# Optimization experiments

Measured on AMD Instinct MI355X. Metric: run time of the kernel, lower is better.

The kernel has to match this reference:

```python
import jax, jax.numpy as jnp
import numpy as np

HIGHEST = jax.lax.Precision.HIGHEST
KEY_CHUNK_SIZE = 4096 * 4  # hard-coded in the module's __call__
HEADS = 8
DIM_HEAD = 64


def _query_chunk_size(num_q: int) -> int:
    # replicates the module's static chunk-size selection
    if num_q % 64 == 0:
        return num_q // 64
    if num_q % 16 == 0:
        return num_q // 16
    if num_q % 4 == 0:
        return num_q // 4
    return num_q


def _me_attention(q, k, v, q_chunk: int, k_chunk: int):
    # q, k, v: (S, H, D) where H here is the flattened batch*heads axis
    S, H, D = q.shape
    num_kv = k.shape[0]
    k_chunk = min(k_chunk, num_kv)
    q = q / jnp.sqrt(jnp.asarray(D, q.dtype))
    kc = k.reshape(-1, k_chunk, H, D)          # (nk, kc, H, D)
    vc = v.reshape(-1, k_chunk, H, v.shape[-1])

    def per_qchunk(qch):  # qch: (qc, H, D)
        def summarize(args):
            kch, vch = args
            s = jnp.einsum('qhd,khd->qhk', qch, kch, precision=HIGHEST)
            m = jax.lax.stop_gradient(jnp.max(s, axis=-1, keepdims=True))
            e = jnp.exp(s - m)
            ev = jnp.einsum('khf,qhk->qhf', vch, e, precision=HIGHEST)
            return ev, e.sum(axis=-1), m[..., 0]
        evs, ews, ms = jax.lax.map(summarize, (kc, vc))  # stacked over key chunks
        gm = jnp.max(ms, axis=0)                # (qc, H) global running max
        sc = jnp.exp(ms - gm)                   # (nk, qc, H) rescale factors
        num = (evs * sc[..., None]).sum(axis=0)
        den = (ews * sc).sum(axis=0)
        return num / den[..., None]

    qs = q.reshape(-1, q_chunk, H, D)
    out = jax.lax.map(per_qchunk, qs)           # (nq, qc, H, F)
    return out.reshape(S, H, -1)


def _forward(hidden_states, w_q, w_k, w_v, w_out, b_out):
    B, S, Dm = hidden_states.shape
    H, dh = HEADS, DIM_HEAD
    q = hidden_states @ w_q
    k = hidden_states @ w_k
    v = hidden_states @ w_v

    def to_heads(t):  # (B,S,H*dh) -> (B*H, S, dh)
        return t.reshape(B, S, H, dh).transpose(0, 2, 1, 3).reshape(B * H, S, dh)

    qs, ks, vs = to_heads(q), to_heads(k), to_heads(v)
    # module transposes to (S, B*H, dh) before memory-efficient attention
    qcs = _query_chunk_size(S)
    attn = _me_attention(qs.transpose(1, 0, 2), ks.transpose(1, 0, 2),
                         vs.transpose(1, 0, 2), qcs, KEY_CHUNK_SIZE)
    attn = attn.transpose(1, 0, 2)  # (B*H, S, dh)
    attn = attn.reshape(B, H, S, dh).transpose(0, 2, 1, 3).reshape(B, S, H * dh)
    return attn @ w_out + b_out


def setup_inputs() -> dict:
    key = jax.random.key(0)
    ks = jax.random.split(key, 6)
    B, S, Dm = 2, 8192, 512
    inner = HEADS * DIM_HEAD  # 512
    return {
        'hidden_states': jax.random.normal(ks[0], (B, S, Dm), dtype=jnp.float32),
        'w_q': jax.random.normal(ks[1], (Dm, inner), dtype=jnp.float32) * 0.02,
        'w_k': jax.random.normal(ks[2], (Dm, inner), dtype=jnp.float32) * 0.02,
        'w_v': jax.random.normal(ks[3], (Dm, inner), dtype=jnp.float32) * 0.02,
        'w_out': jax.random.normal(ks[4], (inner, Dm), dtype=jnp.float32) * 0.02,
        'b_out': jnp.zeros((Dm,), dtype=jnp.float32),
    }


def reference(hidden_states, w_q, w_k, w_v, w_out, b_out):
    return _forward(hidden_states, w_q, w_k, w_v, w_out, b_out)
```

## Files before the change

### kernel.cpp

```cpp
#include <hip/hip_runtime.h>
#include <stdint.h>

typedef unsigned short u16;
typedef __attribute__((ext_vector_type(8))) short short8;
typedef __attribute__((ext_vector_type(4))) short short4v;
typedef __attribute__((ext_vector_type(4))) float f32x4;

#define MFMA16(a, b, c) __builtin_amdgcn_mfma_f32_16x16x16bf16_1k(a, b, c, 0, 0, 0)
#define MFMA32(a, b, c) __builtin_amdgcn_mfma_f32_16x16x32_bf16(a, b, c, 0, 0, 0)

#if __has_builtin(__builtin_amdgcn_exp2f)
#define EXP2F(x) __builtin_amdgcn_exp2f(x)
#else
#define EXP2F(x) exp2f(x)
#endif

#define ASYNC16(G, L)                                                            \
    __builtin_amdgcn_global_load_lds((const __attribute__((address_space(1))) void*)(const void*)(G), \
                                     (__attribute__((address_space(3))) void*)(void*)(L), 16, 0, 0)

__device__ __forceinline__ u16 f2bf(float f) {
    union { float f; uint32_t u; } c; c.f = f;
    uint32_t r = (c.u + 0x7fffu + ((c.u >> 16) & 1u)) >> 16;
    return (u16)r;
}

__global__ __launch_bounds__(256) void k_convert_x(const float* __restrict__ X, u16* __restrict__ Xb) {
    int idx = blockIdx.x * 256 + threadIdx.x;
    float4 v = ((const float4*)X)[idx];
    union { u16 s[4]; uint2 v; } u;
    u.s[0] = f2bf(v.x); u.s[1] = f2bf(v.y); u.s[2] = f2bf(v.z); u.s[3] = f2bf(v.w);
    ((uint2*)Xb)[idx] = u.v;
}

__global__ __launch_bounds__(256) void k_convert_w(const float* __restrict__ W0, const float* __restrict__ W1,
                                                   const float* __restrict__ W2, const float* __restrict__ W3,
                                                   u16* __restrict__ Wt) {
    __shared__ u16 T[64][72];
    const float* W = (blockIdx.z == 0) ? W0 : (blockIdx.z == 1) ? W1 : (blockIdx.z == 2) ? W2 : W3;
    int k0 = blockIdx.x * 64, n0 = blockIdx.y * 64;
    int t = threadIdx.x;
    for (int i = 0; i < 4; i++) {
        int id = t + i * 256;
        int row = id >> 4, c4 = (id & 15) * 4;
        float4 v = *(const float4*)(W + (size_t)(k0 + row) * 512 + n0 + c4);
        union { u16 s[4]; uint2 v; } u;
        u.s[0] = f2bf(v.x); u.s[1] = f2bf(v.y); u.s[2] = f2bf(v.z); u.s[3] = f2bf(v.w);
        *(uint2*)&T[row][c4] = u.v;
    }
    __syncthreads();
    u16* O = Wt + (size_t)blockIdx.z * 512 * 512;
    for (int i = 0; i < 2; i++) {
        int id = t + i * 256;
        int row = id >> 3, c8 = (id & 7) * 8;
        union { u16 s[8]; uint4 v; } tmp;
        for (int j = 0; j < 8; j++) tmp.s[j] = T[c8 + j][row];
        *(uint4*)(O + (size_t)(n0 + row) * 512 + k0 + c8) = tmp.v;
    }
}

__global__ __launch_bounds__(256) void k_gemm_qkv(const u16* __restrict__ X, const u16* __restrict__ Wt,
                                                  u16* __restrict__ Q, u16* __restrict__ K, u16* __restrict__ V) {
    __shared__ u16 As[128][40];
    __shared__ u16 Bs[128][40];
    const int t = threadIdx.x;
    const int wave = t >> 6, lane = t & 63, quad = lane >> 4, l16 = lane & 15;
    const int wm = (wave >> 1) * 64, wn = (wave & 1) * 64;
    const int m0 = blockIdx.x * 128, n0 = blockIdx.y * 128;
    const u16* Bt = Wt + (size_t)blockIdx.z * 262144;
    const f32x4 fz = {0.f, 0.f, 0.f, 0.f};
    f32x4 acc[4][4];
    for (int i = 0; i < 4; i++) for (int j = 0; j < 4; j++) acc[i][j] = fz;
    for (int k0 = 0; k0 < 512; k0 += 32) {
        __syncthreads();
        for (int i = 0; i < 2; i++) {
            int id = t + i * 256;
            int row = id >> 2, c8 = (id & 3) * 8;
            *(uint4*)&As[row][c8] = *(const uint4*)(X + (size_t)(m0 + row) * 512 + k0 + c8);
            *(uint4*)&Bs[row][c8] = *(const uint4*)(Bt + (size_t)(n0 + row) * 512 + k0 + c8);
        }
        __syncthreads();
        short8 af[4], bf[4];
        for (int mt = 0; mt < 4; mt++) af[mt] = *(const short8*)&As[wm + mt * 16 + l16][quad * 8];
        for (int nt = 0; nt < 4; nt++) bf[nt] = *(const short8*)&Bs[wn + nt * 16 + l16][quad * 8];
        for (int mt = 0; mt < 4; mt++)
            for (int nt = 0; nt < 4; nt++)
                acc[mt][nt] = MFMA32(af[mt], bf[nt], acc[mt][nt]);
    }
    const float scale = (blockIdx.z == 0) ? 0.18033688011112042f : 1.0f;
    u16* Out = (blockIdx.z == 0) ? Q : (blockIdx.z == 1) ? K : V;
    for (int mt = 0; mt < 4; mt++)
        for (int nt = 0; nt < 4; nt++)
            for (int r = 0; r < 4; r++) {
                int m = m0 + wm + mt * 16 + quad * 4 + r;
                int n = n0 + wn + nt * 16 + l16;
                int b = m >> 13, s = m & 8191, h = n >> 6, d = n & 63;
                Out[((size_t)((b * 8 + h) * 8192 + s)) * 64 + d] = f2bf(acc[mt][nt][r] * scale);
            }
}

__global__ __launch_bounds__(256) void k_transpose_v(const u16* __restrict__ V, u16* __restrict__ Vt) {
    __shared__ u16 T[64][72];
    int s0 = blockIdx.x * 64, bh = blockIdx.y;
    int t = threadIdx.x;
    for (int i = 0; i < 2; i++) {
        int id = t + i * 256, row = id >> 3, c8 = (id & 7) * 8;
        *(uint4*)&T[row][c8] = *(const uint4*)(V + ((size_t)bh * 8192 + s0 + row) * 64 + c8);
    }
    __syncthreads();
    for (int i = 0; i < 2; i++) {
        int id = t + i * 256, row = id >> 3, c8 = (id & 7) * 8;
        union { u16 s[8]; uint4 v; } tmp;
        for (int j = 0; j < 8; j++) tmp.s[j] = T[c8 + j][row];
        *(uint4*)(Vt + ((size_t)bh * 64 + row) * 8192 + s0 + c8) = tmp.v;
    }
}

__global__ __launch_bounds__(512, 4) void k_flash(const u16* __restrict__ Q, const u16* __restrict__ K,
                                                  const u16* __restrict__ Vt, u16* __restrict__ Attn) {
    __shared__ u16 KsAll[2][4096];
    __shared__ u16 VsAll[2][4096];
    const int t = threadIdx.x;
    const int wave = t >> 6, lane = t & 63, quad = lane >> 4, l16 = lane & 15;
    const int l7 = l16 & 7, q1 = quad >> 1, qlo = quad & 1;
    const int qblk = blockIdx.x, bh = blockIdx.y;
    const int b = bh >> 3, h = bh & 7;
    const int q0g = qblk * 256;
    const int mq = wave * 32;
    const u16* Qb = Q + ((size_t)bh * 8192 + q0g) * 64;
    const u16* Kb = K + (size_t)bh * 8192 * 64;
    const u16* Vb = Vt + (size_t)bh * 64 * 8192;

    const int r0 = t >> 3;
    const int x0 = ((t & 7) ^ (r0 & 7)) * 8;
    const u16* gK0 = Kb + r0 * 64 + x0;
    const u16* gV0 = Vb + (size_t)r0 * 8192 + x0;
    u16* lK = &KsAll[0][0] + t * 8;
    u16* lV = &VsAll[0][0] + t * 8;

    auto prefetch = [&](int it, int buf) {
        ASYNC16(gK0 + it * 4096, lK + buf * 4096);
        ASYNC16(gV0 + it * 64,   lV + buf * 4096);
    };

    short8 qf[2][2];
    for (int mt = 0; mt < 2; mt++)
        for (int ks = 0; ks < 2; ks++)
            qf[mt][ks] = *(const short8*)(Qb + (size_t)(mq + mt * 16 + l16) * 64 + ks * 32 + quad * 8);

    const f32x4 fz = {0.f, 0.f, 0.f, 0.f};
    f32x4 o[2][4];
    float l_i[2] = {0.f, 0.f};
    for (int mt = 0; mt < 2; mt++) for (int nt = 0; nt < 4; nt++) o[mt][nt] = fz;

    prefetch(0, 0);

    auto body = [&](int it, int buf) {
        __syncthreads();
        if (it != 127) prefetch(it + 1, buf ^ 1);
        const u16* KsB = &KsAll[buf][0];
        const u16* VsB = &VsAll[buf][0];

        f32x4 sc[2][4];
        for (int kt = 0; kt < 4; kt++) {
            short8 kf0 = *(const short8*)(KsB + kt * 1024 + l16 * 64 + (((0 * 4 + quad) ^ l7) * 8));
            short8 kf1 = *(const short8*)(KsB + kt * 1024 + l16 * 64 + (((1 * 4 + quad) ^ l7) * 8));
            sc[0][kt] = MFMA32(kf0, qf[0][0], fz);
            sc[1][kt] = MFMA32(kf0, qf[1][0], fz);
            sc[0][kt] = MFMA32(kf1, qf[0][1], sc[0][kt]);
            sc[1][kt] = MFMA32(kf1, qf[1][1], sc[1][kt]);
        }

        short4v pf[2][4];
        for (int mt = 0; mt < 2; mt++)
            for (int kt = 0; kt < 4; kt++) {
                union { float f; uint32_t u; } e0, e1, e2, e3;
                e0.f = EXP2F(sc[mt][kt][0]);
                e1.f = EXP2F(sc[mt][kt][1]);
                e2.f = EXP2F(sc[mt][kt][2]);
                e3.f = EXP2F(sc[mt][kt][3]);
                l_i[mt] += (e0.f + e1.f) + (e2.f + e3.f);
                union { uint32_t u[2]; short4v s; } pk;
                pk.u[0] = __builtin_amdgcn_perm(e1.u, e0.u, 0x07060302);
                pk.u[1] = __builtin_amdgcn_perm(e3.u, e2.u, 0x07060302);
                pf[mt][kt] = pk.s;
            }

        for (int kt = 0; kt < 4; kt++)
            for (int nt = 0; nt < 4; nt++) {
                short4v vf = *(const short4v*)(VsB + nt * 1024 + l16 * 64 + (((kt * 2 + q1) ^ l7) * 8) + qlo * 4);
                o[0][nt] = MFMA16(pf[0][kt], vf, o[0][nt]);
                o[1][nt] = MFMA16(pf[1][kt], vf, o[1][nt]);
            }
    };

    for (int it2 = 0; it2 < 64; it2++) {
        body(2 * it2, 0);
        body(2 * it2 + 1, 1);
    }

    for (int mt = 0; mt < 2; mt++) {
        float l = l_i[mt];
        l += __shfl_xor(l, 16);
        l += __shfl_xor(l, 32);
        float inv = 1.0f / l;
        float invC[4];
        for (int r = 0; r < 4; r++) invC[r] = __shfl(inv, quad * 4 + r);
        for (int nt = 0; nt < 4; nt++)
            for (int r = 0; r < 4; r++) {
                int sg = q0g + mq + mt * 16 + quad * 4 + r;
                int n = h * 64 + nt * 16 + l16;
                Attn[((size_t)(b * 8192 + sg)) * 512 + n] = f2bf(o[mt][nt][r] * invC[r]);
            }
    }
}

__global__ __launch_bounds__(256) void k_gemm_out(const u16* __restrict__ A, const u16* __restrict__ Wot,
                                                  const float* __restrict__ bias, float* __restrict__ Out) {
    __shared__ u16 As[128][40];
    __shared__ u16 Bs[128][40];
    const int t = threadIdx.x;
    const int wave = t >> 6, lane = t & 63, quad = lane >> 4, l16 = lane & 15;
    const int wm = (wave >> 1) * 64, wn = (wave & 1) * 64;
    const int m0 = blockIdx.x * 128, n0 = blockIdx.y * 128;
    const f32x4 fz = {0.f, 0.f, 0.f, 0.f};
    f32x4 acc[4][4];
    for (int i = 0; i < 4; i++) for (int j = 0; j < 4; j++) acc[i][j] = fz;
    for (int k0 = 0; k0 < 512; k0 += 32) {
        __syncthreads();
        for (int i = 0; i < 2; i++) {
            int id = t + i * 256;
            int row = id >> 2, c8 = (id & 3) * 8;
            *(uint4*)&As[row][c8] = *(const uint4*)(A + (size_t)(m0 + row) * 512 + k0 + c8);
            *(uint4*)&Bs[row][c8] = *(const uint4*)(Wot + (size_t)(n0 + row) * 512 + k0 + c8);
        }
        __syncthreads();
        short8 af[4], bf[4];
        for (int mt = 0; mt < 4; mt++) af[mt] = *(const short8*)&As[wm + mt * 16 + l16][quad * 8];
        for (int nt = 0; nt < 4; nt++) bf[nt] = *(const short8*)&Bs[wn + nt * 16 + l16][quad * 8];
        for (int mt = 0; mt < 4; mt++)
            for (int nt = 0; nt < 4; nt++)
                acc[mt][nt] = MFMA32(af[mt], bf[nt], acc[mt][nt]);
    }
    float bv[4];
    for (int nt = 0; nt < 4; nt++) bv[nt] = bias[n0 + wn + nt * 16 + l16];
    for (int mt = 0; mt < 4; mt++)
        for (int nt = 0; nt < 4; nt++)
            for (int r = 0; r < 4; r++) {
                int m = m0 + wm + mt * 16 + quad * 4 + r;
                int n = n0 + wn + nt * 16 + l16;
                Out[(size_t)m * 512 + n] = acc[mt][nt][r] + bv[nt];
            }
}

extern "C" void kernel_launch(void* const* d_in, const int* in_sizes, int n_in,
                              void* d_out, int out_size, void* d_ws, size_t ws_size,
                              hipStream_t stream) {
    const float* X   = (const float*)d_in[0];
    const float* w_q = (const float*)d_in[1];
    const float* w_k = (const float*)d_in[2];
    const float* w_v = (const float*)d_in[3];
    const float* w_o = (const float*)d_in[4];
    const float* b_o = (const float*)d_in[5];
    float* Out = (float*)d_out;

    char* ws = (char*)d_ws;
    u16* Xb   = (u16*)(ws);
    u16* Wt   = (u16*)(ws + 16777216);
    u16* Qd   = (u16*)(ws + 18874368);
    u16* Kd   = (u16*)(ws + 35651584);
    u16* Vd   = (u16*)(ws + 52428800);
    u16* Vtd  = (u16*)(ws + 69206016);
    u16* Attn = Xb;

    hipLaunchKernelGGL(k_convert_x, dim3(8192), dim3(256), 0, stream, X, Xb);
    hipLaunchKernelGGL(k_convert_w, dim3(8, 8, 4), dim3(256), 0, stream, w_q, w_k, w_v, w_o, Wt);
    hipLaunchKernelGGL(k_gemm_qkv, dim3(128, 4, 3), dim3(256), 0, stream, Xb, Wt, Qd, Kd, Vd);
    hipLaunchKernelGGL(k_transpose_v, dim3(128, 16), dim3(256), 0, stream, Vd, Vtd);
    hipLaunchKernelGGL(k_flash, dim3(32, 16), dim3(512), 0, stream, Qd, Kd, Vtd, Attn);
    hipLaunchKernelGGL(k_gemm_out, dim3(128, 4), dim3(256), 0, stream, Attn, Wt + 3 * 262144, b_o, Out);
}
```

Baseline: 437.5 us.

## Use 16x16x32 bf16 MFMA for PV product via permuted K row mapping

Permutes the key rows assigned to each QK^T score tile and changes the K LDS swizzle so each lane's exponentiated scores form a contiguous 8-element bf16 fragment. That lets the P·V product use the K=32 MFMA with 128-bit V loads, halving the MFMA instruction count and the V LDS reads for that stage. In exchange it adds more complex row-index arithmetic and needs the K swizzle and the score layout to agree exactly.

```diff
diff --git a/kernel.cpp b/kernel.cpp
--- a/kernel.cpp
+++ b/kernel.cpp
@@ -122,7 +122,7 @@
     __shared__ u16 VsAll[2][4096];
     const int t = threadIdx.x;
     const int wave = t >> 6, lane = t & 63, quad = lane >> 4, l16 = lane & 15;
-    const int l7 = l16 & 7, q1 = quad >> 1, qlo = quad & 1;
+    const int l7 = l16 & 7;
     const int qblk = blockIdx.x, bh = blockIdx.y;
     const int b = bh >> 3, h = bh & 7;
     const int q0g = qblk * 256;
@@ -131,10 +131,13 @@
     const u16* Kb = K + (size_t)bh * 8192 * 64;
     const u16* Vb = Vt + (size_t)bh * 64 * 8192;
 
+    const int rA = ((l16 & 12) << 1) + (l16 & 3);
+
     const int r0 = t >> 3;
-    const int x0 = ((t & 7) ^ (r0 & 7)) * 8;
-    const u16* gK0 = Kb + r0 * 64 + x0;
-    const u16* gV0 = Vb + (size_t)r0 * 8192 + x0;
+    const int x0K = ((t & 7) ^ ((r0 & 3) | ((r0 & 8) >> 1))) * 8;
+    const int x0V = ((t & 7) ^ (r0 & 7)) * 8;
+    const u16* gK0 = Kb + r0 * 64 + x0K;
+    const u16* gV0 = Vb + (size_t)r0 * 8192 + x0V;
     u16* lK = &KsAll[0][0] + t * 8;
     u16* lV = &VsAll[0][0] + t * 8;
 
@@ -161,36 +164,50 @@
         const u16* KsB = &KsAll[buf][0];
         const u16* VsB = &VsAll[buf][0];
 
-        f32x4 sc[2][4];
-        for (int kt = 0; kt < 4; kt++) {
-            short8 kf0 = *(const short8*)(KsB + kt * 1024 + l16 * 64 + (((0 * 4 + quad) ^ l7) * 8));
-            short8 kf1 = *(const short8*)(KsB + kt * 1024 + l16 * 64 + (((1 * 4 + quad) ^ l7) * 8));
-            sc[0][kt] = MFMA32(kf0, qf[0][0], fz);
-            sc[1][kt] = MFMA32(kf0, qf[1][0], fz);
-            sc[0][kt] = MFMA32(kf1, qf[0][1], sc[0][kt]);
-            sc[1][kt] = MFMA32(kf1, qf[1][1], sc[1][kt]);
+        f32x4 scA[2][2], scB[2][2];
+        for (int kg = 0; kg < 2; kg++) {
+            const u16* KgA = KsB + kg * 2048 + rA * 64;
+            const u16* KgB = KgA + 4 * 64;
+            short8 a0 = *(const short8*)(KgA + ((0 * 4 + quad) ^ l7) * 8);
+            short8 a1 = *(const short8*)(KgA + ((1 * 4 + quad) ^ l7) * 8);
+            short8 b0 = *(const short8*)(KgB + ((0 * 4 + quad) ^ l7) * 8);
+            short8 b1 = *(const short8*)(KgB + ((1 * 4 + quad) ^ l7) * 8);
+            scA[0][kg] = MFMA32(a0, qf[0][0], fz);
+            scA[1][kg] = MFMA32(a0, qf[1][0], fz);
+            scB[0][kg] = MFMA32(b0, qf[0][0], fz);
+            scB[1][kg] = MFMA32(b0, qf[1][0], fz);
+            scA[0][kg] = MFMA32(a1, qf[0][1], scA[0][kg]);
+            scA[1][kg] = MFMA32(a1, qf[1][1], scA[1][kg]);
+            scB[0][kg] = MFMA32(b1, qf[0][1], scB[0][kg]);
+            scB[1][kg] = MFMA32(b1, qf[1][1], scB[1][kg]);
         }
 
-        short4v pf[2][4];
+        short8 pf[2][2];
         for (int mt = 0; mt < 2; mt++)
-            for (int kt = 0; kt < 4; kt++) {
-                union { float f; uint32_t u; } e0, e1, e2, e3;
-                e0.f = EXP2F(sc[mt][kt][0]);
-                e1.f = EXP2F(sc[mt][kt][1]);
-                e2.f = EXP2F(sc[mt][kt][2]);
-                e3.f = EXP2F(sc[mt][kt][3]);
-                l_i[mt] += (e0.f + e1.f) + (e2.f + e3.f);
-                union { uint32_t u[2]; short4v s; } pk;
-                pk.u[0] = __builtin_amdgcn_perm(e1.u, e0.u, 0x07060302);
-                pk.u[1] = __builtin_amdgcn_perm(e3.u, e2.u, 0x07060302);
-                pf[mt][kt] = pk.s;
-            }
-
-        for (int kt = 0; kt < 4; kt++)
+            for (int kg = 0; kg < 2; kg++) {
+                union { float f; uint32_t u; } eA0, eA1, eA2, eA3, eB0, eB1, eB2, eB3;
+                eA0.f = EXP2F(scA[mt][kg][0]);
+                eA1.f = EXP2F(scA[mt][kg][1]);
+                eA2.f = EXP2F(scA[mt][kg][2]);
+                eA3.f = EXP2F(scA[mt][kg][3]);
+                eB0.f = EXP2F(scB[mt][kg][0]);
+                eB1.f = EXP2F(scB[mt][kg][1]);
+                eB2.f = EXP2F(scB[mt][kg][2]);
+                eB3.f = EXP2F(scB[mt][kg][3]);
+                l_i[mt] += ((eA0.f + eA1.f) + (eA2.f + eA3.f)) + ((eB0.f + eB1.f) + (eB2.f + eB3.f));
+                union { uint32_t u[4]; short8 s; } pk;
+                pk.u[0] = __builtin_amdgcn_perm(eA1.u, eA0.u, 0x07060302);
+                pk.u[1] = __builtin_amdgcn_perm(eA3.u, eA2.u, 0x07060302);
+                pk.u[2] = __builtin_amdgcn_perm(eB1.u, eB0.u, 0x07060302);
+                pk.u[3] = __builtin_amdgcn_perm(eB3.u, eB2.u, 0x07060302);
+                pf[mt][kg] = pk.s;
+            }
+
+        for (int kg = 0; kg < 2; kg++)
             for (int nt = 0; nt < 4; nt++) {
-                short4v vf = *(const short4v*)(VsB + nt * 1024 + l16 * 64 + (((kt * 2 + q1) ^ l7) * 8) + qlo * 4);
-                o[0][nt] = MFMA16(pf[0][kt], vf, o[0][nt]);
-                o[1][nt] = MFMA16(pf[1][kt], vf, o[1][nt]);
+                short8 vf = *(const short8*)(VsB + nt * 1024 + l16 * 64 + (((kg * 4 + quad) ^ l7) * 8));
+                o[0][nt] = MFMA32(pf[0][kg], vf, o[0][nt]);
+                o[1][nt] = MFMA32(pf[1][kg], vf, o[1][nt]);
             }
     };
 
```

New measurement: 392.2 us. -10.3%, faster.

## Switch flash attention to 32x32 MFMA tiles and fuse X conversion into QKV GEMM

Applied to the files above, without the earlier changes.

The flash kernel now uses 32x32x16 bf16 MFMAs for both QK^T and PV instead of 16x16 tiles. The K load order is permuted so the score accumulator layout can be packed straight into PV operands without shuffles, and the epilogue is rewritten for the 32x32 layout. Separately, the fp32-to-bf16 conversion of X moves into the QKV GEMM's LDS load, which removes one kernel launch and a round trip through memory. The cost is that X is reread and converted again for each N tile and each of the three projections.

```diff
diff --git a/kernel.cpp b/kernel.cpp
--- a/kernel.cpp
+++ b/kernel.cpp
@@ -3,11 +3,11 @@
 
 typedef unsigned short u16;
 typedef __attribute__((ext_vector_type(8))) short short8;
-typedef __attribute__((ext_vector_type(4))) short short4v;
 typedef __attribute__((ext_vector_type(4))) float f32x4;
-
-#define MFMA16(a, b, c) __builtin_amdgcn_mfma_f32_16x16x16bf16_1k(a, b, c, 0, 0, 0)
+typedef __attribute__((ext_vector_type(16))) float f32x16;
+
 #define MFMA32(a, b, c) __builtin_amdgcn_mfma_f32_16x16x32_bf16(a, b, c, 0, 0, 0)
+#define MFMA3232(a, b, c) __builtin_amdgcn_mfma_f32_32x32x16_bf16(a, b, c, 0, 0, 0)
 
 #if __has_builtin(__builtin_amdgcn_exp2f)
 #define EXP2F(x) __builtin_amdgcn_exp2f(x)
@@ -23,14 +23,6 @@
     union { float f; uint32_t u; } c; c.f = f;
     uint32_t r = (c.u + 0x7fffu + ((c.u >> 16) & 1u)) >> 16;
     return (u16)r;
-}
-
-__global__ __launch_bounds__(256) void k_convert_x(const float* __restrict__ X, u16* __restrict__ Xb) {
-    int idx = blockIdx.x * 256 + threadIdx.x;
-    float4 v = ((const float4*)X)[idx];
-    union { u16 s[4]; uint2 v; } u;
-    u.s[0] = f2bf(v.x); u.s[1] = f2bf(v.y); u.s[2] = f2bf(v.z); u.s[3] = f2bf(v.w);
-    ((uint2*)Xb)[idx] = u.v;
 }
 
 __global__ __launch_bounds__(256) void k_convert_w(const float* __restrict__ W0, const float* __restrict__ W1,
@@ -59,7 +51,7 @@
     }
 }
 
-__global__ __launch_bounds__(256) void k_gemm_qkv(const u16* __restrict__ X, const u16* __restrict__ Wt,
+__global__ __launch_bounds__(256) void k_gemm_qkv(const float* __restrict__ X, const u16* __restrict__ Wt,
                                                   u16* __restrict__ Q, u16* __restrict__ K, u16* __restrict__ V) {
     __shared__ u16 As[128][40];
     __shared__ u16 Bs[128][40];
@@ -76,7 +68,12 @@
         for (int i = 0; i < 2; i++) {
             int id = t + i * 256;
             int row = id >> 2, c8 = (id & 3) * 8;
-            *(uint4*)&As[row][c8] = *(const uint4*)(X + (size_t)(m0 + row) * 512 + k0 + c8);
+            float4 xa = *(const float4*)(X + (size_t)(m0 + row) * 512 + k0 + c8);
+            float4 xb = *(const float4*)(X + (size_t)(m0 + row) * 512 + k0 + c8 + 4);
+            union { u16 s[8]; uint4 v; } ux;
+            ux.s[0] = f2bf(xa.x); ux.s[1] = f2bf(xa.y); ux.s[2] = f2bf(xa.z); ux.s[3] = f2bf(xa.w);
+            ux.s[4] = f2bf(xb.x); ux.s[5] = f2bf(xb.y); ux.s[6] = f2bf(xb.z); ux.s[7] = f2bf(xb.w);
+            *(uint4*)&As[row][c8] = ux.v;
             *(uint4*)&Bs[row][c8] = *(const uint4*)(Bt + (size_t)(n0 + row) * 512 + k0 + c8);
         }
         __syncthreads();
@@ -121,8 +118,9 @@
     __shared__ u16 KsAll[2][4096];
     __shared__ u16 VsAll[2][4096];
     const int t = threadIdx.x;
-    const int wave = t >> 6, lane = t & 63, quad = lane >> 4, l16 = lane & 15;
-    const int l7 = l16 & 7, q1 = quad >> 1, qlo = quad & 1;
+    const int wave = t >> 6, lane = t & 63;
+    const int l32 = lane & 31, hi = lane >> 5;
+    const int s7 = l32 & 7;
     const int qblk = blockIdx.x, bh = blockIdx.y;
     const int b = bh >> 3, h = bh & 7;
     const int q0g = qblk * 256;
@@ -132,9 +130,11 @@
     const u16* Vb = Vt + (size_t)bh * 64 * 8192;
 
     const int r0 = t >> 3;
-    const int x0 = ((t & 7) ^ (r0 & 7)) * 8;
-    const u16* gK0 = Kb + r0 * 64 + x0;
-    const u16* gV0 = Vb + (size_t)r0 * 8192 + x0;
+    const int pr = (r0 & 3) | ((r0 & 4) << 1) | ((r0 & 8) >> 1) | (r0 & 48);
+    const int x0K = ((t & 7) ^ (r0 & 7)) * 8;
+    const int x0V = ((t & 7) ^ (r0 & 7)) * 8;
+    const u16* gK0 = Kb + pr * 64 + x0K;
+    const u16* gV0 = Vb + (size_t)r0 * 8192 + x0V;
     u16* lK = &KsAll[0][0] + t * 8;
     u16* lV = &VsAll[0][0] + t * 8;
 
@@ -143,15 +143,13 @@
         ASYNC16(gV0 + it * 64,   lV + buf * 4096);
     };
 
-    short8 qf[2][2];
-    for (int mt = 0; mt < 2; mt++)
-        for (int ks = 0; ks < 2; ks++)
-            qf[mt][ks] = *(const short8*)(Qb + (size_t)(mq + mt * 16 + l16) * 64 + ks * 32 + quad * 8);
-
-    const f32x4 fz = {0.f, 0.f, 0.f, 0.f};
-    f32x4 o[2][4];
-    float l_i[2] = {0.f, 0.f};
-    for (int mt = 0; mt < 2; mt++) for (int nt = 0; nt < 4; nt++) o[mt][nt] = fz;
+    short8 qf[4];
+    for (int g = 0; g < 4; g++)
+        qf[g] = *(const short8*)(Qb + (size_t)(mq + l32) * 64 + g * 16 + hi * 8);
+
+    const f32x16 fz16 = {};
+    f32x16 o0 = {}, o1 = {};
+    float l_i = 0.f;
 
     prefetch(0, 0);
 
@@ -161,37 +159,47 @@
         const u16* KsB = &KsAll[buf][0];
         const u16* VsB = &VsAll[buf][0];
 
-        f32x4 sc[2][4];
-        for (int kt = 0; kt < 4; kt++) {
-            short8 kf0 = *(const short8*)(KsB + kt * 1024 + l16 * 64 + (((0 * 4 + quad) ^ l7) * 8));
-            short8 kf1 = *(const short8*)(KsB + kt * 1024 + l16 * 64 + (((1 * 4 + quad) ^ l7) * 8));
-            sc[0][kt] = MFMA32(kf0, qf[0][0], fz);
-            sc[1][kt] = MFMA32(kf0, qf[1][0], fz);
-            sc[0][kt] = MFMA32(kf1, qf[0][1], sc[0][kt]);
-            sc[1][kt] = MFMA32(kf1, qf[1][1], sc[1][kt]);
-        }
-
-        short4v pf[2][4];
-        for (int mt = 0; mt < 2; mt++)
-            for (int kt = 0; kt < 4; kt++) {
-                union { float f; uint32_t u; } e0, e1, e2, e3;
-                e0.f = EXP2F(sc[mt][kt][0]);
-                e1.f = EXP2F(sc[mt][kt][1]);
-                e2.f = EXP2F(sc[mt][kt][2]);
-                e3.f = EXP2F(sc[mt][kt][3]);
-                l_i[mt] += (e0.f + e1.f) + (e2.f + e3.f);
-                union { uint32_t u[2]; short4v s; } pk;
-                pk.u[0] = __builtin_amdgcn_perm(e1.u, e0.u, 0x07060302);
-                pk.u[1] = __builtin_amdgcn_perm(e3.u, e2.u, 0x07060302);
-                pf[mt][kt] = pk.s;
-            }
-
-        for (int kt = 0; kt < 4; kt++)
-            for (int nt = 0; nt < 4; nt++) {
-                short4v vf = *(const short4v*)(VsB + nt * 1024 + l16 * 64 + (((kt * 2 + q1) ^ l7) * 8) + qlo * 4);
-                o[0][nt] = MFMA16(pf[0][kt], vf, o[0][nt]);
-                o[1][nt] = MFMA16(pf[1][kt], vf, o[1][nt]);
-            }
+        const u16* K0 = KsB + l32 * 64;
+        const u16* K1 = K0 + 2048;
+        f32x16 s0, s1;
+        s0 = MFMA3232(*(const short8*)(K0 + ((0 + hi) ^ s7) * 8), qf[0], fz16);
+        s0 = MFMA3232(*(const short8*)(K0 + ((2 + hi) ^ s7) * 8), qf[1], s0);
+        s0 = MFMA3232(*(const short8*)(K0 + ((4 + hi) ^ s7) * 8), qf[2], s0);
+        s0 = MFMA3232(*(const short8*)(K0 + ((6 + hi) ^ s7) * 8), qf[3], s0);
+        s1 = MFMA3232(*(const short8*)(K1 + ((0 + hi) ^ s7) * 8), qf[0], fz16);
+        s1 = MFMA3232(*(const short8*)(K1 + ((2 + hi) ^ s7) * 8), qf[1], s1);
+        s1 = MFMA3232(*(const short8*)(K1 + ((4 + hi) ^ s7) * 8), qf[2], s1);
+        s1 = MFMA3232(*(const short8*)(K1 + ((6 + hi) ^ s7) * 8), qf[3], s1);
+
+        union fu { float f; uint32_t u; };
+        uint32_t w[2][8];
+#pragma unroll
+        for (int j = 0; j < 8; j++) {
+            fu a, c; a.f = EXP2F(s0[2 * j]); c.f = EXP2F(s0[2 * j + 1]);
+            l_i += a.f + c.f;
+            w[0][j] = __builtin_amdgcn_perm(c.u, a.u, 0x07060302);
+        }
+#pragma unroll
+        for (int j = 0; j < 8; j++) {
+            fu a, c; a.f = EXP2F(s1[2 * j]); c.f = EXP2F(s1[2 * j + 1]);
+            l_i += a.f + c.f;
+            w[1][j] = __builtin_amdgcn_perm(c.u, a.u, 0x07060302);
+        }
+
+        const u16* V0 = VsB + l32 * 64;
+        const u16* V1 = V0 + 2048;
+#pragma unroll
+        for (int f = 0; f < 4; f++) {
+            union { uint32_t u[4]; short8 s; } pk;
+            pk.u[0] = w[f >> 1][4 * (f & 1) + 0];
+            pk.u[1] = w[f >> 1][4 * (f & 1) + 1];
+            pk.u[2] = w[f >> 1][4 * (f & 1) + 2];
+            pk.u[3] = w[f >> 1][4 * (f & 1) + 3];
+            short8 va = *(const short8*)(V0 + ((2 * f + hi) ^ s7) * 8);
+            short8 vb = *(const short8*)(V1 + ((2 * f + hi) ^ s7) * 8);
+            o0 = MFMA3232(pk.s, va, o0);
+            o1 = MFMA3232(pk.s, vb, o1);
+        }
     };
 
     for (int it2 = 0; it2 < 64; it2++) {
@@ -199,19 +207,16 @@
         body(2 * it2 + 1, 1);
     }
 
-    for (int mt = 0; mt < 2; mt++) {
-        float l = l_i[mt];
-        l += __shfl_xor(l, 16);
-        l += __shfl_xor(l, 32);
-        float inv = 1.0f / l;
-        float invC[4];
-        for (int r = 0; r < 4; r++) invC[r] = __shfl(inv, quad * 4 + r);
-        for (int nt = 0; nt < 4; nt++)
-            for (int r = 0; r < 4; r++) {
-                int sg = q0g + mq + mt * 16 + quad * 4 + r;
-                int n = h * 64 + nt * 16 + l16;
-                Attn[((size_t)(b * 8192 + sg)) * 512 + n] = f2bf(o[mt][nt][r] * invC[r]);
-            }
+    l_i += __shfl_xor(l_i, 32);
+    float inv = 1.0f / l_i;
+#pragma unroll
+    for (int reg = 0; reg < 16; reg++) {
+        int qrow = (reg & 3) + 8 * (reg >> 2) + 4 * hi;
+        float iv = __shfl(inv, qrow);
+        int sg = q0g + mq + qrow;
+        size_t base = ((size_t)(b * 8192 + sg)) * 512 + h * 64;
+        Attn[base + l32]      = f2bf(o0[reg] * iv);
+        Attn[base + 32 + l32] = f2bf(o1[reg] * iv);
     }
 }
 
@@ -265,17 +270,15 @@
     float* Out = (float*)d_out;
 
     char* ws = (char*)d_ws;
-    u16* Xb   = (u16*)(ws);
+    u16* Attn = (u16*)(ws);
     u16* Wt   = (u16*)(ws + 16777216);
     u16* Qd   = (u16*)(ws + 18874368);
     u16* Kd   = (u16*)(ws + 35651584);
     u16* Vd   = (u16*)(ws + 52428800);
     u16* Vtd  = (u16*)(ws + 69206016);
-    u16* Attn = Xb;
-
-    hipLaunchKernelGGL(k_convert_x, dim3(8192), dim3(256), 0, stream, X, Xb);
+
     hipLaunchKernelGGL(k_convert_w, dim3(8, 8, 4), dim3(256), 0, stream, w_q, w_k, w_v, w_o, Wt);
-    hipLaunchKernelGGL(k_gemm_qkv, dim3(128, 4, 3), dim3(256), 0, stream, Xb, Wt, Qd, Kd, Vd);
+    hipLaunchKernelGGL(k_gemm_qkv, dim3(128, 4, 3), dim3(256), 0, stream, X, Wt, Qd, Kd, Vd);
     hipLaunchKernelGGL(k_transpose_v, dim3(128, 16), dim3(256), 0, stream, Vd, Vtd);
     hipLaunchKernelGGL(k_flash, dim3(32, 16), dim3(512), 0, stream, Qd, Kd, Vtd, Attn);
     hipLaunchKernelGGL(k_gemm_out, dim3(128, 4), dim3(256), 0, stream, Attn, Wt + 3 * 262144, b_o, Out);
```

After: 407.6 us. 6.8% less time.
